# Performance work log

Measured on AMD Instinct MI355X. Metric: run time of the kernel, lower is better.

## Reference

```python
import jax, jax.numpy as jnp
import numpy as np

B, T, D, K = 8, 4096, 1024, 3


def setup_inputs() -> dict:
    key = jax.random.key(0)
    k0, k1, k2 = jax.random.split(key, 3)
    x = jax.random.normal(k0, (B, T, D), dtype=jnp.float32)
    lim = 1.0 / np.sqrt(D)
    Wv = jax.random.uniform(k1, (D, D), dtype=jnp.float32, minval=-lim, maxval=lim)
    bv = jnp.zeros((D,), dtype=jnp.float32)
    Wo = jax.random.uniform(k2, (D, D), dtype=jnp.float32, minval=-lim, maxval=lim)
    bo = jnp.zeros((D,), dtype=jnp.float32)
    neighbor_weights = jnp.ones((K,), dtype=jnp.float32) / K
    return {"x": x, "Wv": Wv, "bv": bv, "Wo": Wo, "bo": bo,
            "neighbor_weights": neighbor_weights}


def reference(x, Wv, bv, Wo, bo, neighbor_weights):
    # x: [B, T, D]; faithful translation of the unfold -> Linear -> weighted-sum chain
    k = neighbor_weights.shape[0]
    pad = k // 2
    t = x.shape[1]
    # replicate padding along T (torch F.pad mode='replicate')
    xp = jnp.pad(x, ((0, 0), (pad, pad), (0, 0)), mode='edge')  # [B, T+2*pad, D]
    # sliding windows: [B, T, K, D] (small fixed K loop, not a data-dim loop)
    windows = jnp.stack([xp[:, i:i + t, :] for i in range(k)], axis=2)
    # value projection applied per window element (nn.Linear: x @ W.T + b)
    v = jnp.einsum('btkd,ed->btke', windows, Wv) + bv  # [B, T, K, D]
    # fixed-weight neighbor average
    attended = jnp.einsum('btkd,k->btd', v, neighbor_weights)  # [B, T, D]
    # output projection
    return jnp.einsum('btd,ed->bte', attended, Wo) + bo
```

## Files before the change

### kernel.cpp

```cpp
#include <hip/hip_runtime.h>
#include <stdint.h>
#include <stddef.h>

typedef _Float16 f16_t;
typedef _Float16 f16x4 __attribute__((ext_vector_type(4)));
typedef _Float16 f16x8 __attribute__((ext_vector_type(8)));
typedef float f32x4 __attribute__((ext_vector_type(4)));
typedef float f32x8 __attribute__((ext_vector_type(8)));

#define AS_G __attribute__((address_space(1)))
#define AS_L __attribute__((address_space(3)))

__device__ __forceinline__ void gload_lds16(const void* g, void* l) {
  __builtin_amdgcn_global_load_lds((AS_G void*)g, (AS_L void*)l, 16, 0, 0);
}

#define FENCE() asm volatile("" ::: "memory")
#define BARX()                            \
  do {                                    \
    FENCE();                              \
    __builtin_amdgcn_s_barrier();         \
    FENCE();                              \
  } while (0)
#define VMCNT(n) asm volatile("s_waitcnt vmcnt(" #n ")" ::: "memory")


__global__ __launch_bounds__(256) void prep_fused_kernel(
    const float* __restrict__ X, const float* __restrict__ Wo,
    const float* __restrict__ Wv, const float* __restrict__ bv,
    const float* __restrict__ bo, const float* __restrict__ nw, int Kw,
    f16_t* __restrict__ Xavg, f16_t* __restrict__ WcT, float* __restrict__ bc) {
  __shared__ __align__(16) f16_t sA[128 * 32];
  __shared__ __align__(16) float sWvT[128 * 36];
  __shared__ float smem[256];
  const int b = blockIdx.x;
  const int tid = threadIdx.x;

  if (b < 64) {
    constexpr int K = 1024, NN = 1024;
    const int mt = b & 7, nt = b >> 3;
    const int m0 = mt << 7, n0 = nt << 7;
    const int l = tid & 63, w = tid >> 6;
    const int wr = w >> 1, wc = w & 1;
    const int q = l >> 4;
    const int ka = q << 3;
    const int ar = (wr << 6) + (l & 15);
    const int br = (wc << 6) + (l & 15);
    const int kS = tid >> 3;
    const int cS = (tid & 7) << 4;

    f32x4 acc[4][4];
#pragma unroll
    for (int i = 0; i < 4; ++i)
#pragma unroll
      for (int j = 0; j < 4; ++j) acc[i][j] = f32x4{0.f, 0.f, 0.f, 0.f};

    for (int kt = 0; kt < (K >> 5); ++kt) {
      const int kb = kt << 5;
#pragma unroll
      for (int i = 0; i < 2; ++i) {
        const int u = tid + i * 256;
        const int row = u >> 2, ch = u & 3;
        f32x8 v = *(const f32x8*)(Wo + (size_t)(m0 + row) * K + kb + ch * 8);
        f16x8 h;
#pragma unroll
        for (int e = 0; e < 8; ++e) h[e] = (f16_t)v[e];
        *(f16x8*)(sA + row * 32 + ch * 8) = h;
      }
#pragma unroll
      for (int j = 0; j < 4; ++j) {
        f32x4 v = *(const f32x4*)(Wv + (size_t)(kb + kS) * NN + n0 + cS + 4 * j);
#pragma unroll
        for (int i = 0; i < 4; ++i) sWvT[(cS + 4 * j + i) * 36 + kS] = v[i];
      }
      __syncthreads();
      f16x8 af[4], bfr[4];
#pragma unroll
      for (int m = 0; m < 4; ++m) af[m] = *(const f16x8*)(sA + (ar + (m << 4)) * 32 + ka);
#pragma unroll
      for (int n = 0; n < 4; ++n) {
        f32x4 v0 = *(const f32x4*)(sWvT + (br + (n << 4)) * 36 + ka);
        f32x4 v1 = *(const f32x4*)(sWvT + (br + (n << 4)) * 36 + ka + 4);
#pragma unroll
        for (int e = 0; e < 4; ++e) {
          bfr[n][e] = (f16_t)v0[e];
          bfr[n][e + 4] = (f16_t)v1[e];
        }
      }
#pragma unroll
      for (int m = 0; m < 4; ++m)
#pragma unroll
        for (int n = 0; n < 4; ++n)
          acc[m][n] = __builtin_amdgcn_mfma_f32_16x16x32_f16(af[m], bfr[n], acc[m][n], 0, 0, 0);
      __syncthreads();
    }

    const int orow = q << 2;
    const int ocol = l & 15;
#pragma unroll
    for (int n = 0; n < 4; ++n) {
      const int gn = n0 + (wc << 6) + (n << 4) + ocol;
#pragma unroll
      for (int m = 0; m < 4; ++m) {
        const int gm = m0 + (wr << 6) + (m << 4) + orow;
#pragma unroll
        for (int j = 0; j < 4; ++j)
          WcT[(size_t)(gm + j) * NN + gn] = (f16_t)acc[m][n][j];
      }
    }
  } else if (b < 1088) {
    const int e = b - 64;
    float sw = 0.f;
    for (int k = 0; k < Kw; ++k) sw += nw[k];
    float p = 0.f;
    for (int d = tid; d < 1024; d += 256) p += Wo[(size_t)e * 1024 + d] * bv[d];
    smem[tid] = p;
    __syncthreads();
    for (int s = 128; s > 0; s >>= 1) {
      if (tid < s) smem[tid] += smem[tid + s];
      __syncthreads();
    }
    if (tid == 0) bc[e] = sw * smem[0] + bo[e];
  } else {
    const int T = 4096, D = 1024;
    const int base = (b - 1088) * 8;
    const int t0 = base & (T - 1);
    const int col = tid * 4;
    const float w0 = nw[0], w1 = nw[1], w2 = nw[2];
    const float* xb = X + (size_t)base * D + col;
    f32x4 va = *(const f32x4*)(xb + (t0 == 0 ? 0 : -D));
    f32x4 vb = *(const f32x4*)(xb);
    f16_t* ob = Xavg + (size_t)base * D + col;
#pragma unroll
    for (int g = 0; g < 8; ++g) {
      f32x4 vc;
      if (t0 + g == T - 1) vc = vb;
      else vc = *(const f32x4*)(xb + (size_t)(g + 1) * D);
      f32x4 y = w0 * va + w1 * vb + w2 * vc;
      f16x4 o;
      o.x = (f16_t)y.x; o.y = (f16_t)y.y; o.z = (f16_t)y.z; o.w = (f16_t)y.w;
      *(f16x4*)(ob + (size_t)g * D) = o;
      va = vb;
      vb = vc;
    }
  }
}


__device__ __forceinline__ void stage256(const f16_t* __restrict__ g, int K,
                                         f16_t* ldsOp, int w, int l) {
#pragma unroll
  for (int i = 0; i < 2; ++i) {
    const int f = i * 512 + w * 64 + l;
    const int row = f >> 2;
    const int ch = f & 3;
    const int col = (((ch ^ ((row >> 1) & 3))) << 3);
    gload_lds16(g + (size_t)row * K + col, ldsOp + i * 4096 + w * 512);
  }
}

__global__ __launch_bounds__(512, 2) void gemm256_kernel(const f16_t* __restrict__ A,
                                                         const f16_t* __restrict__ Bt,
                                                         float* __restrict__ C,
                                                         const float* __restrict__ bias,
                                                         int M, int N, int K) {
  __shared__ __align__(16) f16_t lds[4 * 16384];
  const int tid = threadIdx.x;
  const int l = tid & 63;
  const int w = tid >> 6;
  const int wr = w >> 2;
  const int wc = w & 3;
  const int lr = l & 15;
  const int q = l >> 4;

  const int cpx = (int)gridDim.x >> 3;
  const int swzb = ((int)blockIdx.x & 7) * cpx + ((int)blockIdx.x >> 3);
  const int nNT = N >> 8;
  const int mt = swzb / nNT;
  const int nt = swzb % nNT;
  const int m0 = mt << 8;
  const int n0 = nt << 8;

  const f16_t* Apanel = A + (size_t)m0 * K;
  const f16_t* Bpanel = Bt + (size_t)n0 * K;
  const int sw = (q ^ ((lr >> 1) & 3)) << 3;

  f32x4 acc[8][4];
#pragma unroll
  for (int m = 0; m < 8; ++m)
#pragma unroll
    for (int n = 0; n < 4; ++n) acc[m][n] = f32x4{0.f, 0.f, 0.f, 0.f};

  const int nK = K >> 5;

  for (int t = 0; t < 3; ++t) {
    f16_t* buf = lds + (t & 3) * 16384;
    stage256(Apanel + (t << 5), K, buf, w, l);
    stage256(Bpanel + (t << 5), K, buf + 8192, w, l);
  }
  VMCNT(8);
  BARX();

  for (int t = 0; t < nK; ++t) {
    f16_t* sA = lds + (t & 3) * 16384;
    f16_t* sB = sA + 8192;

    {
      const int tn = (t + 3) < nK ? (t + 3) : (nK - 1);
      f16_t* nbuf = lds + ((t + 3) & 3) * 16384;
      stage256(Apanel + ((size_t)tn << 5), K, nbuf, w, l);
      stage256(Bpanel + ((size_t)tn << 5), K, nbuf + 8192, w, l);
    }

    f16x8 bf[4], af[4], ag[4];
#pragma unroll
    for (int n = 0; n < 4; ++n)
      bf[n] = *(const f16x8*)(sB + (((wc << 6) + (n << 4) + lr) << 5) + sw);
#pragma unroll
    for (int m = 0; m < 4; ++m)
      af[m] = *(const f16x8*)(sA + (((wr << 7) + (m << 4) + lr) << 5) + sw);
#pragma unroll
    for (int m = 0; m < 4; ++m)
      ag[m] = *(const f16x8*)(sA + (((wr << 7) + 64 + (m << 4) + lr) << 5) + sw);

    __builtin_amdgcn_s_setprio(1);
#pragma unroll
    for (int m = 0; m < 4; ++m)
#pragma unroll
      for (int n = 0; n < 4; ++n)
        acc[m][n] = __builtin_amdgcn_mfma_f32_16x16x32_f16(af[m], bf[n], acc[m][n], 0, 0, 0);
#pragma unroll
    for (int m = 0; m < 4; ++m)
#pragma unroll
      for (int n = 0; n < 4; ++n)
        acc[m + 4][n] = __builtin_amdgcn_mfma_f32_16x16x32_f16(ag[m], bf[n], acc[m + 4][n], 0, 0, 0);
    __builtin_amdgcn_s_setprio(0);

    VMCNT(8);
    BARX();
  }

  float bs[4];
#pragma unroll
  for (int n = 0; n < 4; ++n) bs[n] = bias[n0 + (wc << 6) + (n << 4) + lr];
#pragma unroll
  for (int m = 0; m < 8; ++m) {
    const int gm = m0 + (wr << 7) + (m << 4) + (q << 2);
#pragma unroll
    for (int j = 0; j < 4; ++j) {
      float* Crow = C + (size_t)(gm + j) * N + n0 + (wc << 6) + lr;
#pragma unroll
      for (int n = 0; n < 4; ++n) Crow[n << 4] = acc[m][n][j] + bs[n];
    }
  }
}


extern "C" void kernel_launch(void* const* d_in, const int* in_sizes, int n_in,
                              void* d_out, int out_size, void* d_ws, size_t ws_size,
                              hipStream_t stream) {
  const float* x = (const float*)d_in[0];
  const float* Wv = (const float*)d_in[1];
  const float* bv = (const float*)d_in[2];
  const float* Wo = (const float*)d_in[3];
  const float* bo = (const float*)d_in[4];
  const float* nw = (const float*)d_in[5];
  float* out = (float*)d_out;

  char* ws = (char*)d_ws;
  f16_t* WcT  = (f16_t*)(ws + (4u << 20));
  float* bc   = (float*)(ws + (6u << 20));
  f16_t* Xavg = (f16_t*)(ws + (8u << 20));

  prep_fused_kernel<<<dim3(5184), dim3(256), 0, stream>>>(
      x, Wo, Wv, bv, bo, nw, in_sizes[5], Xavg, WcT, bc);
  gemm256_kernel<<<dim3(512), dim3(512), 0, stream>>>(
      Xavg, WcT, out, bc, 32768, 1024, 1024);
}
```

Baseline: 145.1 us.

## Restructure GEMM main loop into 8-phase double-buffered schedule with 64-wide K tiles

Replaces the 4-stage, 32-wide K pipeline with a double-buffered 64-wide K tile. Each tile is split into four phases that interleave LDS fragment reads, global-to-LDS staging of the next tile and MFMA sub-blocks, separated by barriers and sched_barrier. The aim is to overlap memory traffic with MFMA work and cut loop overhead per K step. It adds more barriers per tile and a new XOR swizzle, which risks stalls if the phases are imbalanced.

```diff
diff --git a/kernel.cpp b/kernel.cpp
--- a/kernel.cpp
+++ b/kernel.cpp
@@ -23,6 +23,12 @@
     FENCE();                              \
   } while (0)
 #define VMCNT(n) asm volatile("s_waitcnt vmcnt(" #n ")" ::: "memory")
+#define LGKM0() asm volatile("s_waitcnt lgkmcnt(0)" ::: "memory")
+#if defined(__HIP_DEVICE_COMPILE__)
+#define SCHEDB0() __builtin_amdgcn_sched_barrier(0)
+#else
+#define SCHEDB0()
+#endif
 
 
 __global__ __launch_bounds__(256) void prep_fused_kernel(
@@ -147,24 +153,32 @@
 }
 
 
-__device__ __forceinline__ void stage256(const f16_t* __restrict__ g, int K,
-                                         f16_t* ldsOp, int w, int l) {
-#pragma unroll
-  for (int i = 0; i < 2; ++i) {
-    const int f = i * 512 + w * 64 + l;
-    const int row = f >> 2;
-    const int ch = f & 3;
-    const int col = (((ch ^ ((row >> 1) & 3))) << 3);
-    gload_lds16(g + (size_t)row * K + col, ldsOp + i * 4096 + w * 512);
-  }
-}
-
-__global__ __launch_bounds__(512, 2) void gemm256_kernel(const f16_t* __restrict__ A,
-                                                         const f16_t* __restrict__ Bt,
-                                                         float* __restrict__ C,
-                                                         const float* __restrict__ bias,
-                                                         int M, int N, int K) {
-  __shared__ __align__(16) f16_t lds[4 * 16384];
+__device__ __forceinline__ void stageA64(const f16_t* __restrict__ Ap, int K, int kt,
+                                         int c, char* bufA, int w, int l) {
+  const int f = w * 64 + l;
+  const int sub = f >> 3, ch = f & 7;
+  const int grow = ((c & 1) << 7) + ((c >> 1) << 6) + sub;
+  const int gcol = (kt << 6) + ((ch ^ (sub & 7)) << 3);
+  gload_lds16(Ap + (size_t)grow * K + gcol, bufA + c * 8192 + w * 1024);
+}
+
+__device__ __forceinline__ void stageB64(const f16_t* __restrict__ Bp, int K, int kt,
+                                         int c, char* bufB, int w, int l) {
+  const int f = w * 64 + l;
+  const int rr = f >> 3, ch = f & 7;
+  const int wc = ((c & 1) << 1) + (rr >> 5);
+  const int sub = rr & 31;
+  const int grow = (wc << 6) + ((c >> 1) << 5) + sub;
+  const int gcol = (kt << 6) + ((ch ^ (sub & 7)) << 3);
+  gload_lds16(Bp + (size_t)grow * K + gcol, bufB + c * 8192 + w * 1024);
+}
+
+__global__ __launch_bounds__(512, 2) void gemm8p_kernel(const f16_t* __restrict__ A,
+                                                        const f16_t* __restrict__ Bt,
+                                                        float* __restrict__ C,
+                                                        const float* __restrict__ bias,
+                                                        int M, int N, int K) {
+  __shared__ __align__(16) char lds[2 * 65536];
   const int tid = threadIdx.x;
   const int l = tid & 63;
   const int w = tid >> 6;
@@ -183,7 +197,8 @@
 
   const f16_t* Apanel = A + (size_t)m0 * K;
   const f16_t* Bpanel = Bt + (size_t)n0 * K;
-  const int sw = (q ^ ((lr >> 1) & 3)) << 3;
+
+  const int x7 = lr & 7;
 
   f32x4 acc[8][4];
 #pragma unroll
@@ -191,54 +206,95 @@
 #pragma unroll
     for (int n = 0; n < 4; ++n) acc[m][n] = f32x4{0.f, 0.f, 0.f, 0.f};
 
-  const int nK = K >> 5;
-
-  for (int t = 0; t < 3; ++t) {
-    f16_t* buf = lds + (t & 3) * 16384;
-    stage256(Apanel + (t << 5), K, buf, w, l);
-    stage256(Bpanel + (t << 5), K, buf + 8192, w, l);
+  const int nT = K >> 6;
+
+  f16x8 a0[4][2], a1[4][2], b0[2][2], b1[2][2];
+
+#define AREAD(DST, MH, BUF)                                                     \
+  do {                                                                          \
+    const char* p_ = (BUF) + (((MH)*2 + wr) << 13);                             \
+    _Pragma("unroll") for (int mm = 0; mm < 4; ++mm)                            \
+      _Pragma("unroll") for (int kk = 0; kk < 2; ++kk)                          \
+        DST[mm][kk] = *(const f16x8*)(p_ + ((mm * 16 + lr) << 7) +              \
+                                      ((((kk << 2) + q) ^ x7) << 4));           \
+  } while (0)
+#define BREAD(DST, NP, BUF)                                                     \
+  do {                                                                          \
+    const char* p_ = (BUF) + 32768 + ((((NP) << 2) + wc) << 12);                \
+    _Pragma("unroll") for (int nn = 0; nn < 2; ++nn)                            \
+      _Pragma("unroll") for (int kk = 0; kk < 2; ++kk)                          \
+        DST[nn][kk] = *(const f16x8*)(p_ + ((nn * 16 + lr) << 7) +              \
+                                      ((((kk << 2) + q) ^ x7) << 4));           \
+  } while (0)
+#define PH_MFMA(MB, AR, BR, NPB)                                                \
+  do {                                                                          \
+    __builtin_amdgcn_s_setprio(1);                                              \
+    _Pragma("unroll") for (int mm = 0; mm < 4; ++mm)                            \
+      _Pragma("unroll") for (int nn = 0; nn < 2; ++nn) {                        \
+        acc[(MB) + mm][(NPB)*2 + nn] = __builtin_amdgcn_mfma_f32_16x16x32_f16(  \
+            AR[mm][0], BR[nn][0], acc[(MB) + mm][(NPB)*2 + nn], 0, 0, 0);       \
+        acc[(MB) + mm][(NPB)*2 + nn] = __builtin_amdgcn_mfma_f32_16x16x32_f16(  \
+            AR[mm][1], BR[nn][1], acc[(MB) + mm][(NPB)*2 + nn], 0, 0, 0);       \
+      }                                                                         \
+    __builtin_amdgcn_s_setprio(0);                                              \
+  } while (0)
+
+  stageA64(Apanel, K, 0, 0, lds, w, l);
+  stageB64(Bpanel, K, 0, 0, lds + 32768, w, l);
+  stageA64(Apanel, K, 0, 1, lds, w, l);
+  stageB64(Bpanel, K, 0, 1, lds + 32768, w, l);
+  stageA64(Apanel, K, 0, 2, lds, w, l);
+  stageB64(Bpanel, K, 0, 2, lds + 32768, w, l);
+  stageA64(Apanel, K, 0, 3, lds, w, l);
+  stageB64(Bpanel, K, 0, 3, lds + 32768, w, l);
+  VMCNT(4);
+  BARX();
+
+  for (int tt = 0; tt < nT; ++tt) {
+    char* cur = lds + (tt & 1) * 65536;
+    char* nxtA = lds + ((tt + 1) & 1) * 65536;
+    char* nxtB = nxtA + 32768;
+    const int ktn = (tt + 1) < nT ? (tt + 1) : (nT - 1);
+
+    AREAD(a0, 0, cur);
+    BREAD(b0, 0, cur);
+    stageA64(Apanel, K, ktn, 0, nxtA, w, l);
+    stageB64(Bpanel, K, ktn, 0, nxtB, w, l);
+    VMCNT(2);
+    BARX();
+    LGKM0();
+    SCHEDB0();
+    PH_MFMA(0, a0, b0, 0);
+    BARX();
+
+    BREAD(b1, 1, cur);
+    stageA64(Apanel, K, ktn, 1, nxtA, w, l);
+    stageB64(Bpanel, K, ktn, 1, nxtB, w, l);
+    BARX();
+    LGKM0();
+    SCHEDB0();
+    PH_MFMA(0, a0, b1, 1);
+    BARX();
+
+    AREAD(a1, 1, cur);
+    stageA64(Apanel, K, ktn, 2, nxtA, w, l);
+    stageB64(Bpanel, K, ktn, 2, nxtB, w, l);
+    BARX();
+    LGKM0();
+    SCHEDB0();
+    PH_MFMA(4, a1, b0, 0);
+    BARX();
+
+    stageA64(Apanel, K, ktn, 3, nxtA, w, l);
+    stageB64(Bpanel, K, ktn, 3, nxtB, w, l);
+    BARX();
+    PH_MFMA(4, a1, b1, 1);
+    VMCNT(4);
+    BARX();
   }
-  VMCNT(8);
-  BARX();
-
-  for (int t = 0; t < nK; ++t) {
-    f16_t* sA = lds + (t & 3) * 16384;
-    f16_t* sB = sA + 8192;
-
-    {
-      const int tn = (t + 3) < nK ? (t + 3) : (nK - 1);
-      f16_t* nbuf = lds + ((t + 3) & 3) * 16384;
-      stage256(Apanel + ((size_t)tn << 5), K, nbuf, w, l);
-      stage256(Bpanel + ((size_t)tn << 5), K, nbuf + 8192, w, l);
-    }
-
-    f16x8 bf[4], af[4], ag[4];
-#pragma unroll
-    for (int n = 0; n < 4; ++n)
-      bf[n] = *(const f16x8*)(sB + (((wc << 6) + (n << 4) + lr) << 5) + sw);
-#pragma unroll
-    for (int m = 0; m < 4; ++m)
-      af[m] = *(const f16x8*)(sA + (((wr << 7) + (m << 4) + lr) << 5) + sw);
-#pragma unroll
-    for (int m = 0; m < 4; ++m)
-      ag[m] = *(const f16x8*)(sA + (((wr << 7) + 64 + (m << 4) + lr) << 5) + sw);
-
-    __builtin_amdgcn_s_setprio(1);
-#pragma unroll
-    for (int m = 0; m < 4; ++m)
-#pragma unroll
-      for (int n = 0; n < 4; ++n)
-        acc[m][n] = __builtin_amdgcn_mfma_f32_16x16x32_f16(af[m], bf[n], acc[m][n], 0, 0, 0);
-#pragma unroll
-    for (int m = 0; m < 4; ++m)
-#pragma unroll
-      for (int n = 0; n < 4; ++n)
-        acc[m + 4][n] = __builtin_amdgcn_mfma_f32_16x16x32_f16(ag[m], bf[n], acc[m + 4][n], 0, 0, 0);
-    __builtin_amdgcn_s_setprio(0);
-
-    VMCNT(8);
-    BARX();
-  }
+#undef AREAD
+#undef BREAD
+#undef PH_MFMA
 
   float bs[4];
 #pragma unroll
@@ -274,6 +330,6 @@
 
   prep_fused_kernel<<<dim3(5184), dim3(256), 0, stream>>>(
       x, Wo, Wv, bv, bo, nw, in_sizes[5], Xavg, WcT, bc);
-  gemm256_kernel<<<dim3(512), dim3(512), 0, stream>>>(
+  gemm8p_kernel<<<dim3(512), dim3(512), 0, stream>>>(
       Xavg, WcT, out, bc, 32768, 1024, 1024);
 }
```

Measured after the change: 141.0 us. 2.8% less time.
